# Performance work log

Measured on AMD Instinct MI355X. Metric: run time of the kernel, lower is better.

## Reference

```python
import jax, jax.numpy as jnp
import numpy as np

S = 16384   # num src nodes
D = 16384   # num dst nodes
FS = 128    # src feature len
FD = 128    # dst feature len
R = 50.0    # dist threshold (m)
L = 2005.0  # box side so avg degree ~ 32
LN_EPS = 1e-5


def setup_inputs() -> dict:
    rng = np.random.default_rng(0)
    src_pos_np = rng.uniform(0.0, L, (S, 2)).astype(np.float32)
    dst_pos_np = rng.uniform(0.0, L, (D, 2)).astype(np.float32)
    # radius-graph edge construction (data-dependent, done once outside jit)
    es, ed = [], []
    CH = 2048
    for i in range(0, S, CH):
        d = np.linalg.norm(src_pos_np[i:i + CH, None, :] - dst_pos_np[None, :, :], axis=-1)
        si, di = np.nonzero(d <= R)
        es.append((si + i).astype(np.int32))
        ed.append(di.astype(np.int32))
    edge_src_idx = jnp.asarray(np.concatenate(es))
    edge_dst_idx = jnp.asarray(np.concatenate(ed))

    key = jax.random.key(0)
    ks = jax.random.split(key, 12)
    w = lambda k, shape: (jax.random.normal(k, shape, jnp.float32) * 0.02)
    return {
        'src_node_features': jax.random.normal(ks[0], (S, FS), jnp.float32),
        'src_node_pos': jnp.asarray(src_pos_np),
        'dst_node_features': jax.random.normal(ks[1], (D, FD), jnp.float32),
        'dst_node_pos': jnp.asarray(dst_pos_np),
        'src_w': w(ks[2], (FS, FS)), 'src_b': jnp.zeros((FS,), jnp.float32),
        'dst_w': w(ks[3], (FD, FD)), 'dst_b': jnp.zeros((FD,), jnp.float32),
        'dist_w': w(ks[4], (2, FD)), 'dist_b': jnp.zeros((FD,), jnp.float32),
        'edge_w1': w(ks[5], (FS + FD + FD, FD)), 'edge_b1': jnp.zeros((FD,), jnp.float32),
        'edge_w2': w(ks[6], (FD, FD)), 'edge_b2': jnp.zeros((FD,), jnp.float32),
        'ln_g': jnp.ones((FD,), jnp.float32), 'ln_b': jnp.zeros((FD,), jnp.float32),
        'out_w': w(ks[7], (FD, FD)), 'out_b': jnp.zeros((FD,), jnp.float32),
        'edge_src_idx': edge_src_idx,
        'edge_dst_idx': edge_dst_idx,
    }


def reference(src_node_features, src_node_pos, dst_node_features, dst_node_pos,
              src_w, src_b, dst_w, dst_b, dist_w, dist_b,
              edge_w1, edge_b1, edge_w2, edge_b2, ln_g, ln_b, out_w, out_b,
              edge_src_idx, edge_dst_idx):
    # node encoders: Linear + ReLU
    src_enc = jax.nn.relu(src_node_features @ src_w + src_b)   # [S, FS]
    dst_enc = jax.nn.relu(dst_node_features @ dst_w + dst_b)   # [D, FD]
    # gather per-edge
    e_src = src_enc[edge_src_idx]                               # [E, FS]
    e_dst = dst_enc[edge_dst_idx]                               # [E, FD]
    e_dpos = src_node_pos[edge_src_idx] - dst_node_pos[edge_dst_idx]  # [E, 2]
    e_dist = jax.nn.relu(e_dpos @ dist_w + dist_b)              # [E, FD]
    # edge MLP: Linear-ReLU-Linear on concat [E, FS+FD+FD]
    e_in = jnp.concatenate([e_src, e_dist, e_dst], axis=-1)
    e_out = jax.nn.relu(e_in @ edge_w1 + edge_b1) @ edge_w2 + edge_b2  # [E, FD]
    # scatter-add to destination nodes
    agg = dst_enc + jax.ops.segment_sum(e_out, edge_dst_idx, num_segments=D)
    # LayerNorm + ReLU + Linear + residual + ReLU
    mu = jnp.mean(agg, axis=-1, keepdims=True)
    var = jnp.mean(jnp.square(agg - mu), axis=-1, keepdims=True)
    ln = (agg - mu) * jax.lax.rsqrt(var + LN_EPS) * ln_g + ln_b
    h = jax.nn.relu(ln) @ out_w + out_b + dst_node_features
    return jax.nn.relu(h)
```

## Files before the change

kernel.cpp:

```cpp
#include <hip/hip_runtime.h>

typedef unsigned short ushort_t;
typedef unsigned int uint_t;
typedef short bhalf8 __attribute__((ext_vector_type(8)));
typedef float f32x4 __attribute__((ext_vector_type(4)));
typedef float f32x2 __attribute__((ext_vector_type(2)));

#define DEG_CAP 96

__device__ __forceinline__ float b2f(ushort_t u) {
    union { uint_t i; float f; } v; v.i = ((uint_t)u) << 16; return v.f;
}
__device__ __forceinline__ float u2f(uint_t u) {
    union { uint_t i; float f; } v; v.i = u; return v.f;
}
__device__ __forceinline__ ushort_t f2b(float f) {
    union { float f; uint_t i; } v; v.f = f;
    uint_t r = v.i + 0x7fffu + ((v.i >> 16) & 1u);
    return (ushort_t)(r >> 16);
}
__device__ __forceinline__ uint_t f2u(float f) {
    union { float f; uint_t i; } v; v.f = f; return v.i;
}
__device__ __forceinline__ uint_t pack_trunc(float lo, float hi) {
    return (f2u(lo) >> 16) | (f2u(hi) & 0xffff0000u);
}
__device__ __forceinline__ uint_t pack_rhu(float lo, float hi) {
    return ((f2u(lo) + 0x8000u) >> 16) | ((f2u(hi) + 0x8000u) & 0xffff0000u);
}
__device__ __forceinline__ uint_t addpack_trunc(uint_t a, uint_t b) {
    f32x2 A, B;
    A.x = u2f(a << 16); A.y = u2f(a & 0xffff0000u);
    B.x = u2f(b << 16); B.y = u2f(b & 0xffff0000u);
    f32x2 C = A + B;
    return pack_trunc(C.x, C.y);
}

__global__ __launch_bounds__(256) void prep_kernel(
    const float* __restrict__ wsrc, const float* __restrict__ wdst,
    const float* __restrict__ w2,   const float* __restrict__ wout,
    const float* __restrict__ w1,
    ushort_t* __restrict__ msrc, ushort_t* __restrict__ mdst,
    ushort_t* __restrict__ m2,   ushort_t* __restrict__ mout,
    ushort_t* __restrict__ m1a,  ushort_t* __restrict__ m1b,
    ushort_t* __restrict__ m1c,
    const int* __restrict__ esi, const int* __restrict__ edi, int E,
    int* __restrict__ deg, int* __restrict__ bucket,
    int2* __restrict__ edge_sd, int Epad,
    float* __restrict__ hsum, int countB, int zeroB, int Dn)
{
    int b = blockIdx.x, tid = threadIdx.x;
    if (b < 56) {
        const float* ins[7] = { wsrc, wdst, w2, wout, w1, w1 + 16384, w1 + 32768 };
        ushort_t* outs[7]   = { msrc, mdst, m2, mout, m1a, m1b, m1c };
        int mat = b >> 3;
        const float* in = ins[mat];
        ushort_t* out = outs[mat];
        int flat = (b & 7)*256 + tid;
        int nt = flat >> 8, rem = flat & 255;
        int ks = rem >> 6, lane = rem & 63;
        int q = lane >> 4, m = lane & 15;
        #pragma unroll
        for (int j = 0; j < 8; ++j)
            out[flat*8 + j] = f2b(in[(ks*32 + q*8 + j)*128 + nt*16 + m]);
    } else if (b < 56 + countB) {
        int i = (b - 56)*256 + tid;
        if (i < E) {
            int d = edi[i];
            int p = atomicAdd(&deg[d], 1);
            if (p < DEG_CAP) bucket[(size_t)d*DEG_CAP + p] = esi[i];
        }
    } else {
        int zb = b - 56 - countB;
        float4* h4 = (float4*)hsum;
        int total4 = Dn*32;
        for (int i = zb*256 + tid; i < total4; i += zeroB*256)
            h4[i] = make_float4(0.f, 0.f, 0.f, 0.f);
        uint2* e2 = (uint2*)edge_sd;
        for (int i = zb*256 + tid; i < Epad; i += zeroB*256)
            e2[i] = make_uint2(0u, 0xFFFFFFFFu);
    }
}

__global__ __launch_bounds__(256) void enc2_kernel(
    const float* __restrict__ src_feat, const float* __restrict__ dst_feat,
    const ushort_t* __restrict__ msrc, const ushort_t* __restrict__ mdst,
    const ushort_t* __restrict__ m1a,  const ushort_t* __restrict__ m1c,
    const float* __restrict__ src_b,   const float* __restrict__ dst_b,
    const float* __restrict__ b1,
    ushort_t* __restrict__ Csrc, ushort_t* __restrict__ Cdst,
    ushort_t* __restrict__ dst_enc,
    const int* __restrict__ deg, int* __restrict__ P,
    int Dn, int Sb, int Db)
{
    int tid = threadIdx.x, blk = blockIdx.x;

    if (blk == Sb + Db) {
        __shared__ int sums[256];
        int per = Dn >> 8;
        const int4* d4 = (const int4*)(deg + tid*per);
        int4 v[16]; int s = 0;
        #pragma unroll
        for (int k = 0; k < 16; ++k) {
            v[k] = d4[k];
            v[k].x = min(v[k].x, DEG_CAP); v[k].y = min(v[k].y, DEG_CAP);
            v[k].z = min(v[k].z, DEG_CAP); v[k].w = min(v[k].w, DEG_CAP);
            s += v[k].x + v[k].y + v[k].z + v[k].w;
        }
        sums[tid] = s;
        __syncthreads();
        for (int off = 1; off < 256; off <<= 1) {
            int x = (tid >= off) ? sums[tid - off] : 0;
            __syncthreads();
            sums[tid] += x;
            __syncthreads();
        }
        int run = sums[tid] - s;
        int4* n4 = (int4*)(P + tid*per);
        #pragma unroll
        for (int k = 0; k < 16; ++k) {
            int4 o;
            o.x = run; run += v[k].x;
            o.y = run; run += v[k].y;
            o.z = run; run += v[k].z;
            o.w = run; run += v[k].w;
            n4[k] = o;
        }
        return;
    }

    __shared__ ushort_t A_l[64*136];
    __shared__ ushort_t E_l[64*136];
    __shared__ float b_l[128];
    __shared__ float b2_l[128];

    const float* A; const ushort_t *W1m, *W2m; const float* bias; const float* bias2;
    ushort_t *outC, *outEnc; int rowbase;
    if (blk < Sb) { A = src_feat; W1m = msrc; W2m = m1a; bias = src_b;
                    outC = Csrc; outEnc = nullptr; rowbase = blk*64; bias2 = nullptr; }
    else          { A = dst_feat; W1m = mdst; W2m = m1c; bias = dst_b;
                    outC = Cdst; outEnc = dst_enc; rowbase = (blk - Sb)*64; bias2 = b1; }

    const float4* A4 = (const float4*)A;
    for (int i = tid; i < 2048; i += 256) {
        int r = i >> 5, c = i & 31;
        float4 v = A4[(size_t)(rowbase + r)*32 + c];
        uint2 u;
        u.x = pack_trunc(v.x, v.y);
        u.y = pack_trunc(v.z, v.w);
        *(uint2*)(A_l + r*136 + c*4) = u;
    }
    if (tid < 128) { b_l[tid] = bias[tid]; b2_l[tid] = bias2 ? bias2[tid] : 0.f; }
    __syncthreads();

    int lane = tid & 63, w = tid >> 6, q = lane >> 4, m = lane & 15;
    const bhalf8* Wv1 = (const bhalf8*)W1m;
    f32x4 acc[4][2] = {};
    #pragma unroll
    for (int ks = 0; ks < 4; ++ks) {
        bhalf8 bf0 = Wv1[((2*w)*4 + ks)*64 + lane];
        bhalf8 bf1 = Wv1[((2*w+1)*4 + ks)*64 + lane];
        #pragma unroll
        for (int mt = 0; mt < 4; ++mt) {
            bhalf8 a = *(const bhalf8*)(A_l + (mt*16 + m)*136 + ks*32 + q*8);
            acc[mt][0] = __builtin_amdgcn_mfma_f32_16x16x32_bf16(a, bf0, acc[mt][0], 0, 0, 0);
            acc[mt][1] = __builtin_amdgcn_mfma_f32_16x16x32_bf16(a, bf1, acc[mt][1], 0, 0, 0);
        }
    }
    #pragma unroll
    for (int mt = 0; mt < 4; ++mt)
    #pragma unroll
    for (int nt = 0; nt < 2; ++nt)
    #pragma unroll
    for (int reg = 0; reg < 4; ++reg) {
        int col = w*32 + nt*16 + m;
        int row = mt*16 + q*4 + reg;
        E_l[row*136 + col] = f2b(fmaxf(acc[mt][nt][reg] + b_l[col], 0.f));
    }
    __syncthreads();

    if (outEnc) {
        for (int i = tid; i < 1024; i += 256) {
            int r = i >> 4, c = i & 15;
            ((uint4*)outEnc)[(size_t)(rowbase + r)*16 + c] = *(const uint4*)(E_l + r*136 + c*8);
        }
    }

    const bhalf8* Wv2 = (const bhalf8*)W2m;
    f32x4 acc2[4][2] = {};
    #pragma unroll
    for (int ks = 0; ks < 4; ++ks) {
        bhalf8 bf0 = Wv2[((2*w)*4 + ks)*64 + lane];
        bhalf8 bf1 = Wv2[((2*w+1)*4 + ks)*64 + lane];
        #pragma unroll
        for (int mt = 0; mt < 4; ++mt) {
            bhalf8 a = *(const bhalf8*)(E_l + (mt*16 + m)*136 + ks*32 + q*8);
            acc2[mt][0] = __builtin_amdgcn_mfma_f32_16x16x32_bf16(a, bf0, acc2[mt][0], 0, 0, 0);
            acc2[mt][1] = __builtin_amdgcn_mfma_f32_16x16x32_bf16(a, bf1, acc2[mt][1], 0, 0, 0);
        }
    }
    #pragma unroll
    for (int mt = 0; mt < 4; ++mt)
    #pragma unroll
    for (int nt = 0; nt < 2; ++nt)
    #pragma unroll
    for (int reg = 0; reg < 4; ++reg) {
        int col = w*32 + nt*16 + m;
        int row = mt*16 + q*4 + reg;
        A_l[row*136 + col] = f2b(acc2[mt][nt][reg] + b2_l[col]);
    }
    __syncthreads();
    for (int i = tid; i < 1024; i += 256) {
        int r = i >> 4, c = i & 15;
        ((uint4*)outC)[(size_t)(rowbase + r)*16 + c] = *(const uint4*)(A_l + r*136 + c*8);
    }
}

__global__ __launch_bounds__(256) void csr_kernel(
    const int* __restrict__ P, const int* __restrict__ deg,
    const int* __restrict__ bucket, int2* __restrict__ edge_sd, int Dn)
{
    int t = blockIdx.x*256 + threadIdx.x;
    int d = t >> 2, pl = t & 3;
    if (d >= Dn) return;
    int st = P[d];
    int n = min(deg[d], DEG_CAP);
    const int* bk = bucket + (size_t)d*DEG_CAP;
    for (int p = pl; p < n; p += 4)
        edge_sd[st + p] = make_int2(bk[p], d);
}

__global__ __launch_bounds__(512, 8) void edge_kernel(
    const ushort_t* __restrict__ Csrc, const ushort_t* __restrict__ Cdst,
    const float* __restrict__ src_pos, const float* __restrict__ dst_pos,
    const int2* __restrict__ edge_sd, int E, int nTiles,
    const ushort_t* __restrict__ w1bm,
    const float* __restrict__ dist_w, const float* __restrict__ dist_b,
    float* __restrict__ hsum)
{
    __shared__ char pool[18432];
    __shared__ ushort_t G[64*136];
    __shared__ int segd[64];
    __shared__ ushort_t seg16[64];
    __shared__ float2 dxy_l[64];
    __shared__ float dw0_l[128], dw1_l[128], db_l[128];
    __shared__ int nseg_s;

    ushort_t* X  = (ushort_t*)pool;
    ushort_t* Hb = (ushort_t*)pool;

    int tid = threadIdx.x;

    int orig = blockIdx.x;
    int qq = nTiles >> 3, rr = nTiles & 7;
    int xcd = orig & 7, idx = orig >> 3;
    int blk = (xcd < rr ? xcd*(qq + 1) : rr*(qq + 1) + (xcd - rr)*qq) + idx;

    int lane = tid & 63, w = tid >> 6, q = lane >> 4, m = lane & 15;

    const bhalf8* Wv = (const bhalf8*)w1bm;
    bhalf8 wf0 = Wv[(w*4 + 0)*64 + lane];
    bhalf8 wf1 = Wv[(w*4 + 1)*64 + lane];
    bhalf8 wf2 = Wv[(w*4 + 2)*64 + lane];
    bhalf8 wf3 = Wv[(w*4 + 3)*64 + lane];

    int r0 = tid >> 4, c16 = tid & 15;
    const uint4* cs4 = (const uint4*)Csrc;
    const uint4* cd4 = (const uint4*)Cdst;
    int2 e0 = edge_sd[blk*64 + r0];
    int2 e1 = edge_sd[blk*64 + r0 + 32];
    uint4 ga0 = cs4[(size_t)e0.x*16 + c16];
    uint4 gb0 = cd4[(size_t)max(e0.y, 0)*16 + c16];
    uint4 ga1 = cs4[(size_t)e1.x*16 + c16];
    uint4 gb1 = cd4[(size_t)max(e1.y, 0)*16 + c16];

    if (tid < 128) {
        dw0_l[tid] = dist_w[tid];
        dw1_l[tid] = dist_w[128 + tid];
        db_l[tid]  = dist_b[tid];
    }

    if (tid < 64) {
        int2 sd = edge_sd[blk*64 + tid];
        int s = sd.x, d = sd.y;
        float dx = 0.f, dy = 0.f;
        if (d >= 0) {
            float2 sp = ((const float2*)src_pos)[s];
            float2 dp = ((const float2*)dst_pos)[d];
            dx = sp.x - dp.x; dy = sp.y - dp.y;
        }
        dxy_l[tid] = make_float2(dx, dy);
        int dprev = __shfl_up(d, 1);
        bool st = (tid == 0) || (d != dprev);
        unsigned long long smask = __ballot(st);
        int segreg = (int)__popcll(smask << (63 - tid)) - 1;
        seg16[tid] = (ushort_t)segreg;
        if (st) segd[segreg] = (d >= 0) ? d*128 : -1;
        if (tid == 0) nseg_s = (int)__popcll(smask);
    }
    __syncthreads();

    {
        int j2 = (tid & 63)*2;
        int rr2 = tid >> 6;
        float w00 = dw0_l[j2], w01 = dw0_l[j2+1];
        float w10 = dw1_l[j2], w11 = dw1_l[j2+1];
        float bb0 = db_l[j2],  bb1 = db_l[j2+1];
        #pragma unroll
        for (int k = 0; k < 8; ++k) {
            int r = rr2 + k*8;
            float2 dd = dxy_l[r];
            float v0 = fmaxf(fmaf(dd.x, w00, fmaf(dd.y, w10, bb0)), 0.f);
            float v1 = fmaxf(fmaf(dd.x, w01, fmaf(dd.y, w11, bb1)), 0.f);
            *(uint_t*)(X + r*136 + j2) = pack_trunc(v0, v1);
        }
    }

    {
        uint4 u;
        u.x = addpack_trunc(ga0.x, gb0.x);
        u.y = addpack_trunc(ga0.y, gb0.y);
        u.z = addpack_trunc(ga0.z, gb0.z);
        u.w = addpack_trunc(ga0.w, gb0.w);
        *(uint4*)(G + r0*136 + c16*8) = u;
        u.x = addpack_trunc(ga1.x, gb1.x);
        u.y = addpack_trunc(ga1.y, gb1.y);
        u.z = addpack_trunc(ga1.z, gb1.z);
        u.w = addpack_trunc(ga1.w, gb1.w);
        *(uint4*)(G + (r0 + 32)*136 + c16*8) = u;
    }
    __syncthreads();

    f32x4 acc[4] = {};
    #pragma unroll
    for (int mt = 0; mt < 4; ++mt) {
        bhalf8 a0 = *(const bhalf8*)(X + (mt*16 + m)*136 + 0*32 + q*8);
        acc[mt] = __builtin_amdgcn_mfma_f32_16x16x32_bf16(a0, wf0, acc[mt], 0, 0, 0);
        bhalf8 a1 = *(const bhalf8*)(X + (mt*16 + m)*136 + 1*32 + q*8);
        acc[mt] = __builtin_amdgcn_mfma_f32_16x16x32_bf16(a1, wf1, acc[mt], 0, 0, 0);
        bhalf8 a2 = *(const bhalf8*)(X + (mt*16 + m)*136 + 2*32 + q*8);
        acc[mt] = __builtin_amdgcn_mfma_f32_16x16x32_bf16(a2, wf2, acc[mt], 0, 0, 0);
        bhalf8 a3 = *(const bhalf8*)(X + (mt*16 + m)*136 + 3*32 + q*8);
        acc[mt] = __builtin_amdgcn_mfma_f32_16x16x32_bf16(a3, wf3, acc[mt], 0, 0, 0);
    }
    __syncthreads();

    int col = w*16 + m;
    #pragma unroll
    for (int mt = 0; mt < 4; ++mt) {
        int row0 = mt*16 + q*4;
        const ushort_t* gp = G + row0*136 + col;
        float v0 = fmaxf(acc[mt][0] + b2f(gp[0]),   0.f);
        float v1 = fmaxf(acc[mt][1] + b2f(gp[136]), 0.f);
        float v2 = fmaxf(acc[mt][2] + b2f(gp[272]), 0.f);
        float v3 = fmaxf(acc[mt][3] + b2f(gp[408]), 0.f);
        uint2 u;
        u.x = pack_rhu(v0, v1);
        u.y = pack_rhu(v2, v3);
        *(uint2*)(Hb + col*72 + row0) = u;
    }
    __builtin_amdgcn_sched_barrier(0);

    int ns = nseg_s;
    bhalf8 sv0 = *(const bhalf8*)(seg16 + q*8);
    bhalf8 sv1 = *(const bhalf8*)(seg16 + 32 + q*8);
    const ushort_t* hrow = Hb + col*72 + q*8;
    bhalf8 hb0 = *(const bhalf8*)(hrow);
    bhalf8 hb1 = *(const bhalf8*)(hrow + 32);
    const short onebf = (short)0x3f80;
    for (int sb = 0; sb*16 < ns; ++sb) {
        short target = (short)(sb*16 + m);
        bhalf8 a0, a1;
        #pragma unroll
        for (int j = 0; j < 8; ++j) {
            a0[j] = (sv0[j] == target) ? onebf : (short)0;
            a1[j] = (sv1[j] == target) ? onebf : (short)0;
        }
        f32x4 o = {};
        o = __builtin_amdgcn_mfma_f32_16x16x32_bf16(a0, hb0, o, 0, 0, 0);
        o = __builtin_amdgcn_mfma_f32_16x16x32_bf16(a1, hb1, o, 0, 0, 0);
        #pragma unroll
        for (int reg = 0; reg < 4; ++reg) {
            int seg = sb*16 + q*4 + reg;
            if (seg < ns) {
                int ofs = segd[seg];
                if (ofs >= 0) atomicAdd(&hsum[(size_t)ofs + col], o[reg]);
            }
        }
    }
}

__global__ __launch_bounds__(256) void aggfinal16_kernel(
    const float* __restrict__ hsum, const ushort_t* __restrict__ w2m,
    const float* __restrict__ b2, const int* __restrict__ deg,
    const ushort_t* __restrict__ dst_enc, const float* __restrict__ ln_g,
    const float* __restrict__ ln_b, const ushort_t* __restrict__ moutm,
    const float* __restrict__ out_b, const float* __restrict__ dst_feat,
    float* __restrict__ out)
{
    __shared__ ushort_t A_l[16*136];
    __shared__ ushort_t E2[16*136];
    __shared__ float ps[64], ps2[64];
    __shared__ float muv[16], invv[16];
    __shared__ float pb2[128], pg[128], plb[128], pob[128];
    __shared__ int dgl[16];

    int tid = threadIdx.x, blk = blockIdx.x;
    int lane = tid & 63, w = tid >> 6, q = lane >> 4, m = lane & 15;

    if (tid < 128) { pb2[tid] = b2[tid]; pg[tid] = ln_g[tid];
                     plb[tid] = ln_b[tid]; pob[tid] = out_b[tid]; }
    if (tid < 16) dgl[tid] = deg[blk*16 + tid];
    {
        int r = tid >> 4, c = tid & 15;
        const float4* hv4 = (const float4*)hsum;
        size_t base = (size_t)(blk*16 + r)*32 + c*2;
        float4 p0 = hv4[base], p1 = hv4[base + 1];
        uint4 u;
        u.x = pack_trunc(p0.x, p0.y);
        u.y = pack_trunc(p0.z, p0.w);
        u.z = pack_trunc(p1.x, p1.y);
        u.w = pack_trunc(p1.z, p1.w);
        *(uint4*)(A_l + r*136 + c*8) = u;
        *(uint4*)(E2 + r*136 + c*8) = ((const uint4*)dst_enc)[(size_t)(blk*16 + r)*16 + c];
    }
    __syncthreads();

    const bhalf8* Wv2 = (const bhalf8*)w2m;
    f32x4 acc[2] = {};
    #pragma unroll
    for (int ks = 0; ks < 4; ++ks) {
        bhalf8 bf0 = Wv2[((2*w)*4 + ks)*64 + lane];
        bhalf8 bf1 = Wv2[((2*w+1)*4 + ks)*64 + lane];
        bhalf8 a = *(const bhalf8*)(A_l + m*136 + ks*32 + q*8);
        acc[0] = __builtin_amdgcn_mfma_f32_16x16x32_bf16(a, bf0, acc[0], 0, 0, 0);
        acc[1] = __builtin_amdgcn_mfma_f32_16x16x32_bf16(a, bf1, acc[1], 0, 0, 0);
    }
    float y[2][4];
    #pragma unroll
    for (int nt = 0; nt < 2; ++nt)
    #pragma unroll
    for (int reg = 0; reg < 4; ++reg) {
        int col = w*32 + nt*16 + m;
        int rowl = q*4 + reg;
        y[nt][reg] = acc[nt][reg] + (float)dgl[rowl]*pb2[col] + b2f(E2[rowl*136 + col]);
    }
    float s[4], s2[4];
    #pragma unroll
    for (int reg = 0; reg < 4; ++reg) {
        s[reg]  = y[0][reg] + y[1][reg];
        s2[reg] = y[0][reg]*y[0][reg] + y[1][reg]*y[1][reg];
    }
    #pragma unroll
    for (int o = 1; o < 16; o <<= 1) {
        #pragma unroll
        for (int reg = 0; reg < 4; ++reg) {
            s[reg]  += __shfl_xor(s[reg],  o);
            s2[reg] += __shfl_xor(s2[reg], o);
        }
    }
    if (m == 0) {
        #pragma unroll
        for (int reg = 0; reg < 4; ++reg) {
            ps[(q*4 + reg)*4 + w]  = s[reg];
            ps2[(q*4 + reg)*4 + w] = s2[reg];
        }
    }
    __syncthreads();
    if (tid < 16) {
        float su = ps[tid*4] + ps[tid*4+1] + ps[tid*4+2] + ps[tid*4+3];
        float sq = ps2[tid*4] + ps2[tid*4+1] + ps2[tid*4+2] + ps2[tid*4+3];
        float mu = su / 128.f;
        float var = sq / 128.f - mu*mu;
        muv[tid] = mu;
        invv[tid] = 1.0f / sqrtf(var + 1e-5f);
    }
    __syncthreads();
    #pragma unroll
    for (int nt = 0; nt < 2; ++nt)
    #pragma unroll
    for (int reg = 0; reg < 4; ++reg) {
        int col = w*32 + nt*16 + m;
        int rowl = q*4 + reg;
        float v = (y[nt][reg] - muv[rowl])*invv[rowl]*pg[col] + plb[col];
        A_l[rowl*136 + col] = f2b(fmaxf(v, 0.f));
    }
    __syncthreads();

    const bhalf8* Wo = (const bhalf8*)moutm;
    f32x4 acc2[2] = {};
    #pragma unroll
    for (int ks = 0; ks < 4; ++ks) {
        bhalf8 bf0 = Wo[((2*w)*4 + ks)*64 + lane];
        bhalf8 bf1 = Wo[((2*w+1)*4 + ks)*64 + lane];
        bhalf8 a = *(const bhalf8*)(A_l + m*136 + ks*32 + q*8);
        acc2[0] = __builtin_amdgcn_mfma_f32_16x16x32_bf16(a, bf0, acc2[0], 0, 0, 0);
        acc2[1] = __builtin_amdgcn_mfma_f32_16x16x32_bf16(a, bf1, acc2[1], 0, 0, 0);
    }
    #pragma unroll
    for (int nt = 0; nt < 2; ++nt)
    #pragma unroll
    for (int reg = 0; reg < 4; ++reg) {
        int col = w*32 + nt*16 + m;
        size_t grow = (size_t)blk*16 + q*4 + reg;
        float v = acc2[nt][reg] + pob[col] + dst_feat[grow*128 + col];
        out[grow*128 + col] = fmaxf(v, 0.f);
    }
}

extern "C" void kernel_launch(void* const* d_in, const int* in_sizes, int n_in,
                              void* d_out, int out_size, void* d_ws, size_t ws_size,
                              hipStream_t stream)
{
    const float* src_feat = (const float*)d_in[0];
    const float* src_pos  = (const float*)d_in[1];
    const float* dst_feat = (const float*)d_in[2];
    const float* dst_pos  = (const float*)d_in[3];
    const float* src_w    = (const float*)d_in[4];
    const float* src_b    = (const float*)d_in[5];
    const float* dst_w    = (const float*)d_in[6];
    const float* dst_b    = (const float*)d_in[7];
    const float* dist_w   = (const float*)d_in[8];
    const float* dist_b   = (const float*)d_in[9];
    const float* w1       = (const float*)d_in[10];
    const float* b1       = (const float*)d_in[11];
    const float* w2       = (const float*)d_in[12];
    const float* b2       = (const float*)d_in[13];
    const float* ln_g     = (const float*)d_in[14];
    const float* ln_b     = (const float*)d_in[15];
    const float* out_w    = (const float*)d_in[16];
    const float* out_b    = (const float*)d_in[17];
    const int* esi        = (const int*)d_in[18];
    const int* edi        = (const int*)d_in[19];
    int E = in_sizes[18];
    int S = in_sizes[0] / 128;
    int D = in_sizes[2] / 128;
    int nTiles = (E + 63) / 64;
    int Epad = nTiles*64;

    char* ws = (char*)d_ws;
    size_t off = 0;
    auto alloc = [&](size_t bytes) { char* p = ws + off; off += (bytes + 511) & ~(size_t)511; return p; };
    ushort_t* Csrc    = (ushort_t*)alloc((size_t)S*128*2);
    ushort_t* Cdst    = (ushort_t*)alloc((size_t)D*128*2);
    ushort_t* dst_enc = (ushort_t*)alloc((size_t)D*128*2);
    float*    hsum    = (float*)   alloc((size_t)D*128*4);
    ushort_t* t_src   = (ushort_t*)alloc(128*128*2);
    ushort_t* t_dst   = (ushort_t*)alloc(128*128*2);
    ushort_t* t_w2    = (ushort_t*)alloc(128*128*2);
    ushort_t* t_out   = (ushort_t*)alloc(128*128*2);
    ushort_t* t_1a    = (ushort_t*)alloc(128*128*2);
    ushort_t* t_1b    = (ushort_t*)alloc(128*128*2);
    ushort_t* t_1c    = (ushort_t*)alloc(128*128*2);
    int*      deg     = (int*)     alloc((size_t)D*4);
    int*      P       = (int*)     alloc((size_t)D*4);
    int*      bucket  = (int*)     alloc((size_t)D*DEG_CAP*4);
    int2*     edge_sd = (int2*)    alloc((size_t)Epad*8);

    hipMemsetAsync(deg, 0, (size_t)D*4, stream);

    int countB = (E + 255)/256;
    int zeroB = 256;
    prep_kernel<<<56 + countB + zeroB, 256, 0, stream>>>(
        src_w, dst_w, w2, out_w, w1,
        t_src, t_dst, t_w2, t_out, t_1a, t_1b, t_1c,
        esi, edi, E, deg, bucket, edge_sd, Epad, hsum, countB, zeroB, D);

    int Sb = S/64, Db = D/64;
    enc2_kernel<<<Sb + Db + 1, 256, 0, stream>>>(
        src_feat, dst_feat, t_src, t_dst, t_1a, t_1c, src_b, dst_b, b1,
        Csrc, Cdst, dst_enc, deg, P, D, Sb, Db);

    csr_kernel<<<(D*4 + 255)/256, 256, 0, stream>>>(P, deg, bucket, edge_sd, D);

    edge_kernel<<<nTiles, 512, 0, stream>>>(
        Csrc, Cdst, src_pos, dst_pos, edge_sd, E, nTiles,
        t_1b, dist_w, dist_b, hsum);

    aggfinal16_kernel<<<D/16, 256, 0, stream>>>(
        hsum, t_w2, b2, deg, dst_enc, ln_g, ln_b,
        t_out, out_b, dst_feat, (float*)d_out);
}
```

Baseline: 198.0 us.

## Build CSR by atomic fill, fold G add into MFMA, drop XCD remap

Replaces the per-destination bucket array and its CSR copy kernel with a counting-sort pass: the degree histogram produces offsets that are duplicated into a cursor array, and a per-edge fill kernel scatters edges using atomic cursors. This removes the large bucket buffer and its extra pass. In the edge kernel, the gathered G term is added through an extra MFMA with an identity fragment instead of scalar LDS reads and adds. The XCD-aware block remapping is also removed, and the bf16 pack helpers now use v_perm. The atomic fill makes edge order within a segment nondeterministic, and an extra MFMA per tile is added.

```diff
diff --git a/kernel.cpp b/kernel.cpp
--- a/kernel.cpp
+++ b/kernel.cpp
@@ -23,17 +23,15 @@
     union { float f; uint_t i; } v; v.f = f; return v.i;
 }
 __device__ __forceinline__ uint_t pack_trunc(float lo, float hi) {
-    return (f2u(lo) >> 16) | (f2u(hi) & 0xffff0000u);
+    return __builtin_amdgcn_perm(f2u(hi), f2u(lo), 0x07060302u);
 }
 __device__ __forceinline__ uint_t pack_rhu(float lo, float hi) {
-    return ((f2u(lo) + 0x8000u) >> 16) | ((f2u(hi) + 0x8000u) & 0xffff0000u);
+    return __builtin_amdgcn_perm(f2u(hi) + 0x8000u, f2u(lo) + 0x8000u, 0x07060302u);
 }
 __device__ __forceinline__ uint_t addpack_trunc(uint_t a, uint_t b) {
-    f32x2 A, B;
-    A.x = u2f(a << 16); A.y = u2f(a & 0xffff0000u);
-    B.x = u2f(b << 16); B.y = u2f(b & 0xffff0000u);
-    f32x2 C = A + B;
-    return pack_trunc(C.x, C.y);
+    float lo = u2f(a << 16) + u2f(b << 16);
+    float hi = u2f(a & 0xffff0000u) + u2f(b & 0xffff0000u);
+    return __builtin_amdgcn_perm(f2u(hi), f2u(lo), 0x07060302u);
 }
 
 __global__ __launch_bounds__(256) void prep_kernel(
@@ -44,8 +42,8 @@
     ushort_t* __restrict__ m2,   ushort_t* __restrict__ mout,
     ushort_t* __restrict__ m1a,  ushort_t* __restrict__ m1b,
     ushort_t* __restrict__ m1c,
-    const int* __restrict__ esi, const int* __restrict__ edi, int E,
-    int* __restrict__ deg, int* __restrict__ bucket,
+    const int* __restrict__ edi, int E,
+    int* __restrict__ deg,
     int2* __restrict__ edge_sd, int Epad,
     float* __restrict__ hsum, int countB, int zeroB, int Dn)
 {
@@ -65,11 +63,7 @@
             out[flat*8 + j] = f2b(in[(ks*32 + q*8 + j)*128 + nt*16 + m]);
     } else if (b < 56 + countB) {
         int i = (b - 56)*256 + tid;
-        if (i < E) {
-            int d = edi[i];
-            int p = atomicAdd(&deg[d], 1);
-            if (p < DEG_CAP) bucket[(size_t)d*DEG_CAP + p] = esi[i];
-        }
+        if (i < E) atomicAdd(&deg[edi[i]], 1);
     } else {
         int zb = b - 56 - countB;
         float4* h4 = (float4*)hsum;
@@ -90,7 +84,7 @@
     const float* __restrict__ b1,
     ushort_t* __restrict__ Csrc, ushort_t* __restrict__ Cdst,
     ushort_t* __restrict__ dst_enc,
-    const int* __restrict__ deg, int* __restrict__ P,
+    const int* __restrict__ deg, int* __restrict__ P, int* __restrict__ Pc,
     int Dn, int Sb, int Db)
 {
     int tid = threadIdx.x, blk = blockIdx.x;
@@ -117,6 +111,7 @@
         }
         int run = sums[tid] - s;
         int4* n4 = (int4*)(P + tid*per);
+        int4* c4 = (int4*)(Pc + tid*per);
         #pragma unroll
         for (int k = 0; k < 16; ++k) {
             int4 o;
@@ -125,6 +120,7 @@
             o.z = run; run += v[k].z;
             o.w = run; run += v[k].w;
             n4[k] = o;
+            c4[k] = o;
         }
         return;
     }
@@ -216,24 +212,22 @@
     }
 }
 
-__global__ __launch_bounds__(256) void csr_kernel(
-    const int* __restrict__ P, const int* __restrict__ deg,
-    const int* __restrict__ bucket, int2* __restrict__ edge_sd, int Dn)
+__global__ __launch_bounds__(256) void fill_kernel(
+    const int* __restrict__ esi, const int* __restrict__ edi, int E,
+    const int* __restrict__ P, int* __restrict__ Pc,
+    int2* __restrict__ edge_sd)
 {
-    int t = blockIdx.x*256 + threadIdx.x;
-    int d = t >> 2, pl = t & 3;
-    if (d >= Dn) return;
-    int st = P[d];
-    int n = min(deg[d], DEG_CAP);
-    const int* bk = bucket + (size_t)d*DEG_CAP;
-    for (int p = pl; p < n; p += 4)
-        edge_sd[st + p] = make_int2(bk[p], d);
+    int i = blockIdx.x*256 + threadIdx.x;
+    if (i >= E) return;
+    int d = edi[i];
+    int p = atomicAdd(&Pc[d], 1);
+    if (p - P[d] < DEG_CAP) edge_sd[p] = make_int2(esi[i], d);
 }
 
 __global__ __launch_bounds__(512, 8) void edge_kernel(
     const ushort_t* __restrict__ Csrc, const ushort_t* __restrict__ Cdst,
     const float* __restrict__ src_pos, const float* __restrict__ dst_pos,
-    const int2* __restrict__ edge_sd, int E, int nTiles,
+    const int2* __restrict__ edge_sd,
     const ushort_t* __restrict__ w1bm,
     const float* __restrict__ dist_w, const float* __restrict__ dist_b,
     float* __restrict__ hsum)
@@ -249,13 +243,7 @@
     ushort_t* X  = (ushort_t*)pool;
     ushort_t* Hb = (ushort_t*)pool;
 
-    int tid = threadIdx.x;
-
-    int orig = blockIdx.x;
-    int qq = nTiles >> 3, rr = nTiles & 7;
-    int xcd = orig & 7, idx = orig >> 3;
-    int blk = (xcd < rr ? xcd*(qq + 1) : rr*(qq + 1) + (xcd - rr)*qq) + idx;
-
+    int tid = threadIdx.x, blk = blockIdx.x;
     int lane = tid & 63, w = tid >> 6, q = lane >> 4, m = lane & 15;
 
     const bhalf8* Wv = (const bhalf8*)w1bm;
@@ -263,6 +251,13 @@
     bhalf8 wf1 = Wv[(w*4 + 1)*64 + lane];
     bhalf8 wf2 = Wv[(w*4 + 2)*64 + lane];
     bhalf8 wf3 = Wv[(w*4 + 3)*64 + lane];
+
+    int p_id = (w & 1)*16;
+    int win = (w >> 1)*32;
+    bhalf8 iden;
+    #pragma unroll
+    for (int j = 0; j < 8; ++j)
+        iden[j] = (short)((q*8 + j == p_id + m) ? 0x3f80 : 0);
 
     int r0 = tid >> 4, c16 = tid & 15;
     const uint4* cs4 = (const uint4*)Csrc;
@@ -331,9 +326,12 @@
     }
     __syncthreads();
 
-    f32x4 acc[4] = {};
+    f32x4 acc[4];
     #pragma unroll
     for (int mt = 0; mt < 4; ++mt) {
+        f32x4 z = {};
+        bhalf8 g = *(const bhalf8*)(G + (mt*16 + m)*136 + win + q*8);
+        acc[mt] = __builtin_amdgcn_mfma_f32_16x16x32_bf16(g, iden, z, 0, 0, 0);
         bhalf8 a0 = *(const bhalf8*)(X + (mt*16 + m)*136 + 0*32 + q*8);
         acc[mt] = __builtin_amdgcn_mfma_f32_16x16x32_bf16(a0, wf0, acc[mt], 0, 0, 0);
         bhalf8 a1 = *(const bhalf8*)(X + (mt*16 + m)*136 + 1*32 + q*8);
@@ -349,11 +347,10 @@
     #pragma unroll
     for (int mt = 0; mt < 4; ++mt) {
         int row0 = mt*16 + q*4;
-        const ushort_t* gp = G + row0*136 + col;
-        float v0 = fmaxf(acc[mt][0] + b2f(gp[0]),   0.f);
-        float v1 = fmaxf(acc[mt][1] + b2f(gp[136]), 0.f);
-        float v2 = fmaxf(acc[mt][2] + b2f(gp[272]), 0.f);
-        float v3 = fmaxf(acc[mt][3] + b2f(gp[408]), 0.f);
+        float v0 = fmaxf(acc[mt][0], 0.f);
+        float v1 = fmaxf(acc[mt][1], 0.f);
+        float v2 = fmaxf(acc[mt][2], 0.f);
+        float v3 = fmaxf(acc[mt][3], 0.f);
         uint2 u;
         u.x = pack_rhu(v0, v1);
         u.y = pack_rhu(v2, v3);
@@ -554,7 +551,7 @@
     ushort_t* t_1c    = (ushort_t*)alloc(128*128*2);
     int*      deg     = (int*)     alloc((size_t)D*4);
     int*      P       = (int*)     alloc((size_t)D*4);
-    int*      bucket  = (int*)     alloc((size_t)D*DEG_CAP*4);
+    int*      Pc      = (int*)     alloc((size_t)D*4);
     int2*     edge_sd = (int2*)    alloc((size_t)Epad*8);
 
     hipMemsetAsync(deg, 0, (size_t)D*4, stream);
@@ -564,17 +561,18 @@
     prep_kernel<<<56 + countB + zeroB, 256, 0, stream>>>(
         src_w, dst_w, w2, out_w, w1,
         t_src, t_dst, t_w2, t_out, t_1a, t_1b, t_1c,
-        esi, edi, E, deg, bucket, edge_sd, Epad, hsum, countB, zeroB, D);
+        edi, E, deg, edge_sd, Epad, hsum, countB, zeroB, D);
 
     int Sb = S/64, Db = D/64;
     enc2_kernel<<<Sb + Db + 1, 256, 0, stream>>>(
         src_feat, dst_feat, t_src, t_dst, t_1a, t_1c, src_b, dst_b, b1,
-        Csrc, Cdst, dst_enc, deg, P, D, Sb, Db);
-
-    csr_kernel<<<(D*4 + 255)/256, 256, 0, stream>>>(P, deg, bucket, edge_sd, D);
+        Csrc, Cdst, dst_enc, deg, P, Pc, D, Sb, Db);
+
+    fill_kernel<<<(E + 255)/256, 256, 0, stream>>>(
+        esi, edi, E, P, Pc, edge_sd);
 
     edge_kernel<<<nTiles, 512, 0, stream>>>(
-        Csrc, Cdst, src_pos, dst_pos, edge_sd, E, nTiles,
+        Csrc, Cdst, src_pos, dst_pos, edge_sd,
         t_1b, dist_w, dist_b, hsum);
 
     aggfinal16_kernel<<<D/16, 256, 0, stream>>>(
```

Measured after the change: 216.0 us. 1.09x slower.
